# Kernel tuning notes

Hardware: AMD Instinct MI355X
Metric: run time of the kernel (lower is better)

Reference implementation:

```python
import jax, jax.numpy as jnp
import numpy as np

NUM_HEADS = 16
HEAD_DIM = 64
HIDDEN = NUM_HEADS * HEAD_DIM  # 1024


def get_rel_pos(q_size, k_size, rel_pos):
    # q_size == k_size here and rel_pos already has 2*size-1 rows, so the
    # F.interpolate(mode='linear') resize in the original is an identity.
    # relative_coords = q - k + (k_size - 1)  (scale factors are 1.0)
    coords = jnp.arange(q_size)[:, None] - jnp.arange(k_size)[None, :] + (k_size - 1)
    return rel_pos[coords]  # [q_size, k_size, head_dim]


def setup_inputs() -> dict:
    key = jax.random.key(0)
    ks = jax.random.split(key, 7)
    B, H, W = 4, 56, 28
    inp = {
        "hidden_states": jax.random.normal(ks[0], (B, H, W, HIDDEN), jnp.float32),
        "qkv_w": jax.random.normal(ks[1], (3 * HIDDEN, HIDDEN), jnp.float32) * 0.02,
        "qkv_b": jax.random.normal(ks[2], (3 * HIDDEN,), jnp.float32) * 0.02,
        "proj_w": jax.random.normal(ks[3], (HIDDEN, HIDDEN), jnp.float32) * 0.02,
        "proj_b": jax.random.normal(ks[4], (HIDDEN,), jnp.float32) * 0.02,
        "rel_pos_h": jax.random.normal(ks[5], (2 * H - 1, HEAD_DIM), jnp.float32) * 0.02,
        "rel_pos_w": jax.random.normal(ks[6], (2 * W - 1, HEAD_DIM), jnp.float32) * 0.02,
    }
    return inp


def reference(hidden_states, qkv_w, qkv_b, proj_w, proj_b, rel_pos_h, rel_pos_w):
    B, H, W, C = hidden_states.shape
    N = H * W
    scale = HEAD_DIM ** -0.5

    # qkv projection -> [3, B*heads, N, head_dim]
    qkv = hidden_states @ qkv_w.T + qkv_b
    qkv = qkv.reshape(B, N, 3, NUM_HEADS, HEAD_DIM).transpose(2, 0, 3, 1, 4)
    qkv = qkv.reshape(3, B * NUM_HEADS, N, HEAD_DIM)
    query, key_, value = qkv[0], qkv[1], qkv[2]

    # scaled dot-product scores, fully materialized as in the original
    attn = jnp.einsum('bqd,bkd->bqk', query * scale, key_)  # [B*heads, N, N]

    # decomposed relative position bias
    Rh = get_rel_pos(H, H, rel_pos_h)  # [H, H, d]
    Rw = get_rel_pos(W, W, rel_pos_w)  # [W, W, d]
    q_r = query.reshape(B * NUM_HEADS, H, W, HEAD_DIM)
    rel_h = jnp.einsum('bhwc,hkc->bhwk', q_r, Rh)  # [B*heads, H, W, H]
    rel_w = jnp.einsum('bhwc,wkc->bhwk', q_r, Rw)  # [B*heads, H, W, W]
    attn = attn.reshape(B * NUM_HEADS, H, W, H, W)
    attn = attn + rel_h[:, :, :, :, None] + rel_w[:, :, :, None, :]
    attn = attn.reshape(B * NUM_HEADS, N, N)

    attn = jax.nn.softmax(attn.astype(jnp.float32), axis=-1).astype(query.dtype)

    out = jnp.einsum('bqk,bkd->bqd', attn, value)
    out = out.reshape(B, NUM_HEADS, H, W, HEAD_DIM).transpose(0, 2, 3, 1, 4)
    out = out.reshape(B, H, W, C)
    out = out @ proj_w.T + proj_b
    return out
```

## Files before the change

kernel.cpp:

```cpp
#include <hip/hip_runtime.h>
#include <hip/hip_bf16.h>
#include <stdint.h>

typedef __bf16 bf16;
typedef __bf16 bf16x2 __attribute__((ext_vector_type(2)));
typedef __bf16 bf16x4 __attribute__((ext_vector_type(4)));
typedef __bf16 bf16x8 __attribute__((ext_vector_type(8)));
typedef float f32x4 __attribute__((ext_vector_type(4)));

#define AS1 __attribute__((address_space(1)))
#define AS3 __attribute__((address_space(3)))

static __device__ __forceinline__ void async_cp16(const bf16* g, bf16* l) {
    __builtin_amdgcn_global_load_lds((const AS1 void*)g, (AS3 void*)l, 16, 0, 0);
}

static __device__ __forceinline__ bf16x4 cvt4(f32x4 v) {
    bf16x4 r;
    r[0] = (bf16)v[0]; r[1] = (bf16)v[1]; r[2] = (bf16)v[2]; r[3] = (bf16)v[3];
    return r;
}

static __device__ __forceinline__ float fast_exp2(float x) {
#if __has_builtin(__builtin_amdgcn_exp2f)
    return __builtin_amdgcn_exp2f(x);
#else
    return __expf(x * 0.69314718056f);
#endif
}

__global__ __launch_bounds__(256) void cvt_kernel(
    const float* __restrict__ src, bf16* __restrict__ dst, int n4) {
    int i = blockIdx.x * 256 + threadIdx.x;
    const int stride = gridDim.x * 256;
    for (; i < n4; i += stride)
        ((bf16x4*)dst)[i] = cvt4(((const f32x4*)src)[i]);
}


#define QKV_EPILOGUE()                                                        \
    for (int nt = 0; nt < 4; nt++) {                                          \
        const int n_ = n0 + wn + nt * 16 + lm;                                \
        const float bv = bias[n_];                                            \
        const int s = n_ >> 10, rem = n_ & 1023;                              \
        const int h = rem >> 6, d = rem & 63;                                 \
        const float qsc = (s == 0) ? 0.18033688011112042f : 1.0f;             \
        for (int mt = 0; mt < 4; mt++) {                                      \
            for (int r = 0; r < 4; r++) {                                     \
                const int m_ = m0 + wm + mt * 16 + quad * 4 + r;              \
                const int b = m_ / 1568;                                      \
                const int pix = m_ - b * 1568;                                \
                const int g = b * 16 + h;                                     \
                const bf16 v = (bf16)((acc[mt][nt][r] + bv) * qsc);           \
                if (s == 0)      Qb[((size_t)g * 1568 + pix) * 64 + d] = v;   \
                else if (s == 1) Kb[((size_t)g * 1568 + pix) * 64 + d] = v;   \
                else {                                                        \
                    const int lk = pix & 31;                                  \
                    const int ppix = (pix & ~31) | ((lk & 15) << 1) | (lk >> 4); \
                    Vt[((size_t)g * 64 + d) * 1568 + ppix] = v;               \
                }                                                             \
            }                                                                 \
        }                                                                     \
    }

__global__ __launch_bounds__(256) void qkv_gemm_bf16(
    const bf16* __restrict__ A, const bf16* __restrict__ W,
    const float* __restrict__ bias, bf16* __restrict__ Qb,
    bf16* __restrict__ Kb, bf16* __restrict__ Vt) {
    __shared__ bf16 As[128 * 32];
    __shared__ bf16 Bs[128 * 32];
    const int t = threadIdx.x;
    const int wid = t >> 6, lane = t & 63;
    const int m0 = blockIdx.x * 128, n0 = blockIdx.y * 128;
    const int wm = (wid & 1) * 64, wn = (wid >> 1) * 64;
    const int r_i = lane >> 2, c8 = (lane & 3) * 8;
    const int lm = lane & 15, quad = lane >> 4;

    f32x4 acc[4][4] = {};
    for (int k0 = 0; k0 < 1024; k0 += 32) {
        __syncthreads();
        for (int i = 0; i < 2; i++) {
            const int blk = wid * 2 + i;
            async_cp16(A + (size_t)(m0 + blk * 16 + r_i) * 1024 + k0 + c8, As + blk * 512);
            async_cp16(W + (size_t)(n0 + blk * 16 + r_i) * 1024 + k0 + c8, Bs + blk * 512);
        }
        __syncthreads();
        bf16x8 af[4], bfr[4];
        for (int x = 0; x < 4; x++) {
            af[x]  = *(const bf16x8*)&As[(wm + x * 16 + lm) * 32 + quad * 8];
            bfr[x] = *(const bf16x8*)&Bs[(wn + x * 16 + lm) * 32 + quad * 8];
        }
        for (int mt = 0; mt < 4; mt++)
            for (int nt = 0; nt < 4; nt++)
                acc[mt][nt] = __builtin_amdgcn_mfma_f32_16x16x32_bf16(af[mt], bfr[nt], acc[mt][nt], 0, 0, 0);
    }
    QKV_EPILOGUE()
}

__global__ __launch_bounds__(256) void qkv_gemm_f32(
    const float* __restrict__ A, const float* __restrict__ W,
    const float* __restrict__ bias, bf16* __restrict__ Qb,
    bf16* __restrict__ Kb, bf16* __restrict__ Vt) {
    __shared__ bf16 As[128 * 32];
    __shared__ bf16 Bs[128 * 32];
    const int t = threadIdx.x;
    const int wid = t >> 6, lane = t & 63;
    const int m0 = blockIdx.x * 128, n0 = blockIdx.y * 128;
    const int wm = (wid & 1) * 64, wn = (wid >> 1) * 64;
    const int lm = lane & 15, quad = lane >> 4;

    f32x4 acc[4][4] = {};
    for (int k0 = 0; k0 < 1024; k0 += 32) {
        __syncthreads();
        for (int i = 0; i < 4; i++) {
            const int idx = t + i * 256;
            const int row = idx >> 3, c4 = (idx & 7) * 4;
            const f32x4 av = *(const f32x4*)&A[(size_t)(m0 + row) * 1024 + k0 + c4];
            const f32x4 wv = *(const f32x4*)&W[(size_t)(n0 + row) * 1024 + k0 + c4];
            *(bf16x4*)&As[row * 32 + c4] = cvt4(av);
            *(bf16x4*)&Bs[row * 32 + c4] = cvt4(wv);
        }
        __syncthreads();
        bf16x8 af[4], bfr[4];
        for (int x = 0; x < 4; x++) {
            af[x]  = *(const bf16x8*)&As[(wm + x * 16 + lm) * 32 + quad * 8];
            bfr[x] = *(const bf16x8*)&Bs[(wn + x * 16 + lm) * 32 + quad * 8];
        }
        for (int mt = 0; mt < 4; mt++)
            for (int nt = 0; nt < 4; nt++)
                acc[mt][nt] = __builtin_amdgcn_mfma_f32_16x16x32_bf16(af[mt], bfr[nt], acc[mt][nt], 0, 0, 0);
    }
    QKV_EPILOGUE()
}

__global__ __launch_bounds__(256) void flash_attn(
    const bf16* __restrict__ Qb, const bf16* __restrict__ Kb,
    const bf16* __restrict__ Vt, const float* __restrict__ rph,
    const float* __restrict__ rpw, bf16* __restrict__ AO) {
    const int x = blockIdx.x;
    const int xcd = x & 7, j = x >> 3;
    const int g = xcd * 8 + j / 25;
    const int qblk = j - (j / 25) * 25;
    const int q0 = qblk * 64;
    const int hqb = q0 / 28;

    __shared__ __align__(16) char smem[51712];
    float* Th = (float*)smem;
    float* Tw = (float*)(smem + 15360);
    const char* ThC = (const char*)smem;
    const char* TwC = (const char*)(smem + 15360);
    char* B   = smem + 30208;
    bf16* Qs  = (bf16*)B;
    bf16* RPs = (bf16*)B;
    char* KsC = B;
    char* VsC = B + 8192;
    bf16* Ps  = (bf16*)(B + 16384);

    const int t = threadIdx.x, wid = t >> 6, lane = t & 63;
    const int lm = lane & 15, quad = lane >> 4;
    const int qbase_l = wid * 16 + quad * 4;
    const int swz = (lm & 7) << 4;

    for (int c = t; c < 512; c += 256) {
        const int row = c >> 3, col = (c & 7) * 8;
        const int qg = min(q0 + row, 1567);
        *(bf16x8*)&Qs[row * 72 + col] =
            *(const bf16x8*)&Qb[((size_t)g * 1568 + qg) * 64 + col];
    }
    __syncthreads();
    const int qrow_l = wid * 16 + lm;
    const bf16x8 qf0 = *(const bf16x8*)&Qs[qrow_l * 72 + quad * 8];
    const bf16x8 qf1 = *(const bf16x8*)&Qs[qrow_l * 72 + 32 + quad * 8];

    int thbB[4], twbB[4];
#pragma unroll
    for (int r = 0; r < 4; r++) {
        const int qg = min(q0 + qbase_l + r, 1567);
        const int hq = qg / 28, wq = qg - hq * 28;
        thbB[r] = ((qbase_l + r) * 60 + (hq - hqb) + 55) * 4;
        twbB[r] = ((qbase_l + r) * 58 + wq + 27) * 4;
    }

    bf16x8 kreg[2], vreg[2];
#pragma unroll
    for (int i = 0; i < 2; i++) {
        const int idx = (i << 8) + t;
        kreg[i] = *(const bf16x8*)&Kb[((size_t)g * 1568 + (idx >> 3)) * 64 + ((idx & 7) << 3)];
        vreg[i] = *(const bf16x8*)&Vt[((size_t)g * 64 + (idx >> 3)) * 1568 + ((idx & 7) << 3)];
    }
    __syncthreads();

    for (int c = t; c < 1024; c += 256) {
        const int row = c >> 4, col = (c & 15) * 4;
        const int rg = min(hqb + row, 110);
        *(bf16x4*)&RPs[row * 72 + col] = cvt4(*(const f32x4*)&rph[rg * 64 + col]);
    }
    __syncthreads();
    f32x4 acch[4];
#pragma unroll
    for (int nt = 0; nt < 4; nt++) {
        const bf16x8 b0 = *(const bf16x8*)&RPs[(nt * 16 + lm) * 72 + quad * 8];
        const bf16x8 b1 = *(const bf16x8*)&RPs[(nt * 16 + lm) * 72 + 32 + quad * 8];
        f32x4 a = {};
        a = __builtin_amdgcn_mfma_f32_16x16x32_bf16(qf0, b0, a, 0, 0, 0);
        a = __builtin_amdgcn_mfma_f32_16x16x32_bf16(qf1, b1, a, 0, 0, 0);
        acch[nt] = a;
    }
    __syncthreads();

    for (int c = t; c < 1024; c += 256) {
        const int row = c >> 4, col = (c & 15) * 4;
        const int rg = min(row, 54);
        *(bf16x4*)&RPs[row * 72 + col] = cvt4(*(const f32x4*)&rpw[rg * 64 + col]);
    }
#pragma unroll
    for (int nt = 0; nt < 4; nt++) {
        const int c = nt * 16 + lm;
        if (c < 59) {
#pragma unroll
            for (int r = 0; r < 4; r++)
                Th[(qbase_l + r) * 60 + c] = acch[nt][r] * 8.0f - 14.4269504f;
        }
    }
    __syncthreads();
#pragma unroll
    for (int nt = 0; nt < 4; nt++) {
        const bf16x8 b0 = *(const bf16x8*)&RPs[(nt * 16 + lm) * 72 + quad * 8];
        const bf16x8 b1 = *(const bf16x8*)&RPs[(nt * 16 + lm) * 72 + 32 + quad * 8];
        f32x4 a = {};
        a = __builtin_amdgcn_mfma_f32_16x16x32_bf16(qf0, b0, a, 0, 0, 0);
        a = __builtin_amdgcn_mfma_f32_16x16x32_bf16(qf1, b1, a, 0, 0, 0);
        const int c = nt * 16 + lm;
        if (c < 55) {
#pragma unroll
            for (int r = 0; r < 4; r++)
                Tw[(qbase_l + r) * 58 + c] = a[r] * 8.0f;
        }
    }

    f32x4 o[4] = {};
    f32x4 lsum = {};
    bf16x8 ones;
#pragma unroll
    for (int i = 0; i < 8; i++) ones[i] = (bf16)1.0f;

    int hkB[4], wkB[4];
#pragma unroll
    for (int f = 0; f < 4; f++) {
        const int k = f * 16 + lm;
        const int hk = k / 28;
        hkB[f] = hk * 4;
        wkB[f] = (k - hk * 28) * 4;
    }
    bf16* Pw = &Ps[wid * 640];

    for (int kt = 0; kt < 25; kt++) {
        f32x4 s[4];
#pragma unroll
        for (int f = 0; f < 2; f++)
#pragma unroll
            for (int r = 0; r < 4; r++)
                s[f][r] = *(const float*)(ThC + (thbB[r] - hkB[f]))
                        + *(const float*)(TwC + (twbB[r] - wkB[f]));
        if (kt < 24) {
#pragma unroll
            for (int f = 2; f < 4; f++)
#pragma unroll
                for (int r = 0; r < 4; r++)
                    s[f][r] = *(const float*)(ThC + (thbB[r] - hkB[f]))
                            + *(const float*)(TwC + (twbB[r] - wkB[f]));
        } else {
#pragma unroll
            for (int f = 2; f < 4; f++)
#pragma unroll
                for (int r = 0; r < 4; r++)
                    s[f][r] = -30000.0f;
        }

        __syncthreads();
#pragma unroll
        for (int i = 0; i < 2; i++) {
            const int idx = (i << 8) + t;
            const int row = idx >> 3;
            const int cb = (((idx & 7) << 4) ^ ((row & 7) << 4));
            *(bf16x8*)(KsC + row * 128 + cb) = kreg[i];
            *(bf16x8*)(VsC + row * 128 + cb) = vreg[i];
        }
        {
            const int kb = min(kt + 1, 24) << 6;
#pragma unroll
            for (int i = 0; i < 2; i++) {
                const int idx = (i << 8) + t;
                const int krow = min(kb + (idx >> 3), 1567);
                kreg[i] = *(const bf16x8*)&Kb[((size_t)g * 1568 + krow) * 64 + ((idx & 7) << 3)];
                const int vcol = min(kb + ((idx & 7) << 3), 1560);
                vreg[i] = *(const bf16x8*)&Vt[((size_t)g * 64 + (idx >> 3)) * 1568 + vcol];
            }
        }
        __syncthreads();

        __builtin_amdgcn_s_setprio(1);
#pragma unroll
        for (int f = 0; f < 4; f++) {
            const char* rp = KsC + (f * 16 + lm) * 128;
            const int x0 = (quad * 16) ^ swz;
            const bf16x8 ka = *(const bf16x8*)(rp + x0);
            const bf16x8 kb2 = *(const bf16x8*)(rp + (x0 ^ 64));
            s[f] = __builtin_amdgcn_mfma_f32_16x16x32_bf16(qf0, ka, s[f], 0, 0, 0);
            s[f] = __builtin_amdgcn_mfma_f32_16x16x32_bf16(qf1, kb2, s[f], 0, 0, 0);
        }
        __builtin_amdgcn_s_setprio(0);

#pragma unroll
        for (int f = 0; f < 4; f++) {
            wkB[f] += 32; hkB[f] += 8;
            if (wkB[f] >= 112) { wkB[f] -= 112; hkB[f] += 4; }
        }

#pragma unroll
        for (int h = 0; h < 2; h++) {
#pragma unroll
            for (int r = 0; r < 4; r++) {
                const float p0 = fast_exp2(s[2 * h][r]);
                const float p1 = fast_exp2(s[2 * h + 1][r]);
                bf16x2 pp; pp[0] = (bf16)p0; pp[1] = (bf16)p1;
                *(bf16x2*)&Pw[(quad * 4 + r) * 40 + lm * 2] = pp;
            }
            __asm__ volatile("s_waitcnt lgkmcnt(0)" ::: "memory");
            const bf16x8 pf = *(const bf16x8*)&Pw[lm * 40 + quad * 8];
            lsum = __builtin_amdgcn_mfma_f32_16x16x32_bf16(pf, ones, lsum, 0, 0, 0);
            __builtin_amdgcn_s_setprio(1);
#pragma unroll
            for (int dt = 0; dt < 4; dt++) {
                const bf16x8 vf = *(const bf16x8*)(VsC + (dt * 16 + lm) * 128 +
                                                   (((h << 6) + quad * 16) ^ swz));
                o[dt] = __builtin_amdgcn_mfma_f32_16x16x32_bf16(pf, vf, o[dt], 0, 0, 0);
            }
            __builtin_amdgcn_s_setprio(0);
        }
    }

    if (q0 + wid * 16 < 1568) {
        const int bo = g >> 4, hh = g & 15;
#pragma unroll
        for (int r = 0; r < 4; r++) {
            const float inv = 1.0f / lsum[r];
            const size_t base = ((size_t)bo * 1568 + q0 + qbase_l + r) * 1024 + hh * 64;
#pragma unroll
            for (int dt = 0; dt < 4; dt++)
                AO[base + dt * 16 + lm] = (bf16)(o[dt][r] * inv);
        }
    }
}

__global__ __launch_bounds__(256) void proj_gemm_bf16(
    const bf16* __restrict__ A, const bf16* __restrict__ W,
    const float* __restrict__ bias, float* __restrict__ out) {
    __shared__ bf16 As[128 * 32];
    __shared__ bf16 Bs[128 * 32];
    const int t = threadIdx.x;
    const int wid = t >> 6, lane = t & 63;
    const int m0 = blockIdx.x * 128, n0 = blockIdx.y * 128;
    const int wm = (wid & 1) * 64, wn = (wid >> 1) * 64;
    const int r_i = lane >> 2, c8 = (lane & 3) * 8;
    const int lm = lane & 15, quad = lane >> 4;

    f32x4 acc[4][4] = {};
    for (int k0 = 0; k0 < 1024; k0 += 32) {
        __syncthreads();
        for (int i = 0; i < 2; i++) {
            const int blk = wid * 2 + i;
            async_cp16(A + (size_t)(m0 + blk * 16 + r_i) * 1024 + k0 + c8, As + blk * 512);
            async_cp16(W + (size_t)(n0 + blk * 16 + r_i) * 1024 + k0 + c8, Bs + blk * 512);
        }
        __syncthreads();
        bf16x8 af[4], bfr[4];
        for (int x = 0; x < 4; x++) {
            af[x]  = *(const bf16x8*)&As[(wm + x * 16 + lm) * 32 + quad * 8];
            bfr[x] = *(const bf16x8*)&Bs[(wn + x * 16 + lm) * 32 + quad * 8];
        }
        for (int mt = 0; mt < 4; mt++)
            for (int nt = 0; nt < 4; nt++)
                acc[mt][nt] = __builtin_amdgcn_mfma_f32_16x16x32_bf16(af[mt], bfr[nt], acc[mt][nt], 0, 0, 0);
    }
    for (int nt = 0; nt < 4; nt++) {
        const int n_ = n0 + wn + nt * 16 + lm;
        const float bv = bias[n_];
        for (int mt = 0; mt < 4; mt++)
            for (int r = 0; r < 4; r++) {
                const int m_ = m0 + wm + mt * 16 + quad * 4 + r;
                out[(size_t)m_ * 1024 + n_] = acc[mt][nt][r] + bv;
            }
    }
}

__global__ __launch_bounds__(256) void proj_gemm_f32(
    const bf16* __restrict__ A, const float* __restrict__ W,
    const float* __restrict__ bias, float* __restrict__ out) {
    __shared__ bf16 As[128 * 32];
    __shared__ bf16 Bs[128 * 32];
    const int t = threadIdx.x;
    const int wid = t >> 6, lane = t & 63;
    const int m0 = blockIdx.x * 128, n0 = blockIdx.y * 128;
    const int wm = (wid & 1) * 64, wn = (wid >> 1) * 64;
    const int r_i = lane >> 2, c8 = (lane & 3) * 8;
    const int lm = lane & 15, quad = lane >> 4;

    f32x4 acc[4][4] = {};
    for (int k0 = 0; k0 < 1024; k0 += 32) {
        __syncthreads();
        for (int i = 0; i < 2; i++) {
            const int blk = wid * 2 + i;
            async_cp16(A + (size_t)(m0 + blk * 16 + r_i) * 1024 + k0 + c8, As + blk * 512);
        }
        for (int i = 0; i < 4; i++) {
            const int idx = t + i * 256;
            const int row = idx >> 3, c4 = (idx & 7) * 4;
            const f32x4 wv = *(const f32x4*)&W[(size_t)(n0 + row) * 1024 + k0 + c4];
            *(bf16x4*)&Bs[row * 32 + c4] = cvt4(wv);
        }
        __syncthreads();
        bf16x8 af[4], bfr[4];
        for (int x = 0; x < 4; x++) {
            af[x]  = *(const bf16x8*)&As[(wm + x * 16 + lm) * 32 + quad * 8];
            bfr[x] = *(const bf16x8*)&Bs[(wn + x * 16 + lm) * 32 + quad * 8];
        }
        for (int mt = 0; mt < 4; mt++)
            for (int nt = 0; nt < 4; nt++)
                acc[mt][nt] = __builtin_amdgcn_mfma_f32_16x16x32_bf16(af[mt], bfr[nt], acc[mt][nt], 0, 0, 0);
    }
    for (int nt = 0; nt < 4; nt++) {
        const int n_ = n0 + wn + nt * 16 + lm;
        const float bv = bias[n_];
        for (int mt = 0; mt < 4; mt++)
            for (int r = 0; r < 4; r++) {
                const int m_ = m0 + wm + mt * 16 + quad * 4 + r;
                out[(size_t)m_ * 1024 + n_] = acc[mt][nt][r] + bv;
            }
    }
}

extern "C" void kernel_launch(void* const* d_in, const int* in_sizes, int n_in,
                              void* d_out, int out_size, void* d_ws, size_t ws_size,
                              hipStream_t stream) {
    const float* hs     = (const float*)d_in[0];
    const float* qkv_w  = (const float*)d_in[1];
    const float* qkv_b  = (const float*)d_in[2];
    const float* proj_w = (const float*)d_in[3];
    const float* proj_b = (const float*)d_in[4];
    const float* rph    = (const float*)d_in[5];
    const float* rpw    = (const float*)d_in[6];
    float* out = (float*)d_out;

    const size_t GQ = (size_t)64 * 1568 * 64;
    const size_t N_HS = (size_t)6272 * 1024;
    const size_t N_QW = (size_t)3072 * 1024;
    const size_t N_PW = (size_t)1024 * 1024;
    bf16* Qb = (bf16*)d_ws;
    bf16* Kb = Qb + GQ;
    bf16* Vt = Kb + GQ;
    bf16* AO = Vt + GQ;
    bf16* hs_bf    = AO + GQ;
    bf16* qkvw_bf  = hs_bf + N_HS;
    bf16* projw_bf = qkvw_bf + N_QW;
    const size_t need = (4 * GQ + N_HS + N_QW + N_PW) * sizeof(bf16);

    if (ws_size >= need) {
        cvt_kernel<<<512, 256, 0, stream>>>(hs, hs_bf, (int)(N_HS / 4));
        cvt_kernel<<<512, 256, 0, stream>>>(qkv_w, qkvw_bf, (int)(N_QW / 4));
        cvt_kernel<<<256, 256, 0, stream>>>(proj_w, projw_bf, (int)(N_PW / 4));
        qkv_gemm_bf16<<<dim3(49, 24), 256, 0, stream>>>(hs_bf, qkvw_bf, qkv_b, Qb, Kb, Vt);
        flash_attn<<<1600, 256, 0, stream>>>(Qb, Kb, Vt, rph, rpw, AO);
        proj_gemm_bf16<<<dim3(49, 8), 256, 0, stream>>>(AO, projw_bf, proj_b, out);
    } else {
        qkv_gemm_f32<<<dim3(49, 24), 256, 0, stream>>>(hs, qkv_w, qkv_b, Qb, Kb, Vt);
        flash_attn<<<1600, 256, 0, stream>>>(Qb, Kb, Vt, rph, rpw, AO);
        proj_gemm_f32<<<dim3(49, 8), 256, 0, stream>>>(AO, proj_w, proj_b, out);
    }
}
```

Before: 337.9 us.

## Compute relative-position bias via one-hot MFMA instead of LDS gathers

Replaces the per-element LDS gathers of the height and width relative-position tables with an extra MFMA per key fragment. A precomputed one-hot key matrix (Kone) selects the right bias from a per-query bf16 table holding 28 width entries plus 4 height entries. This moves scalar LDS loads and adds onto the matrix cores. In exchange, the bias is rounded to bf16, which costs some precision. It also adds a small setup kernel, an extra global and LDS stream per tile, and one more sync in the prologue.

```diff
diff --git a/kernel.cpp b/kernel.cpp
--- a/kernel.cpp
+++ b/kernel.cpp
@@ -35,6 +35,25 @@
     const int stride = gridDim.x * 256;
     for (; i < n4; i += stride)
         ((bf16x4*)dst)[i] = cvt4(((const f32x4*)src)[i]);
+}
+
+__global__ __launch_bounds__(256) void build_kone(bf16* __restrict__ Kone) {
+    const int idx = blockIdx.x * 256 + threadIdx.x;
+    if (idx >= 6400) return;
+    const int key = idx >> 2, chunk = idx & 3;
+    const int hk = key / 28;
+    const int wk = key - hk * 28;
+    const int kt = key >> 6;
+    const int ha = (kt << 6) / 28;
+    const int jw = 27 - wk;
+    const int jh = 31 - (hk - ha);
+    bf16x8 v;
+#pragma unroll
+    for (int e = 0; e < 8; e++) {
+        const int j = chunk * 8 + e;
+        v[e] = (j == jw || j == jh) ? (bf16)1.0f : (bf16)0.0f;
+    }
+    *(bf16x8*)&Kone[key * 32 + chunk * 8] = v;
 }
 
 
@@ -136,7 +155,8 @@
 __global__ __launch_bounds__(256) void flash_attn(
     const bf16* __restrict__ Qb, const bf16* __restrict__ Kb,
     const bf16* __restrict__ Vt, const float* __restrict__ rph,
-    const float* __restrict__ rpw, bf16* __restrict__ AO) {
+    const float* __restrict__ rpw, const bf16* __restrict__ Kone,
+    bf16* __restrict__ AO) {
     const int x = blockIdx.x;
     const int xcd = x & 7, j = x >> 3;
     const int g = xcd * 8 + j / 25;
@@ -144,17 +164,18 @@
     const int q0 = qblk * 64;
     const int hqb = q0 / 28;
 
-    __shared__ __align__(16) char smem[51712];
-    float* Th = (float*)smem;
-    float* Tw = (float*)(smem + 15360);
+    __shared__ __align__(16) char smem[45312];
+    float* Th  = (float*)smem;
     const char* ThC = (const char*)smem;
-    const char* TwC = (const char*)(smem + 15360);
-    char* B   = smem + 30208;
+    bf16* TwS = (bf16*)(smem + 15616);
+    char* B   = smem + 19712;
     bf16* Qs  = (bf16*)B;
     bf16* RPs = (bf16*)B;
+    float* TwF = (float*)(B + 9216);
     char* KsC = B;
     char* VsC = B + 8192;
-    bf16* Ps  = (bf16*)(B + 16384);
+    bf16* KoneS = (bf16*)(B + 16384);
+    bf16* Ps  = (bf16*)(B + 20480);
 
     const int t = threadIdx.x, wid = t >> 6, lane = t & 63;
     const int lm = lane & 15, quad = lane >> 4;
@@ -172,22 +193,18 @@
     const bf16x8 qf0 = *(const bf16x8*)&Qs[qrow_l * 72 + quad * 8];
     const bf16x8 qf1 = *(const bf16x8*)&Qs[qrow_l * 72 + 32 + quad * 8];
 
-    int thbB[4], twbB[4];
-#pragma unroll
-    for (int r = 0; r < 4; r++) {
-        const int qg = min(q0 + qbase_l + r, 1567);
-        const int hq = qg / 28, wq = qg - hq * 28;
-        thbB[r] = ((qbase_l + r) * 60 + (hq - hqb) + 55) * 4;
-        twbB[r] = ((qbase_l + r) * 58 + wq + 27) * 4;
-    }
-
-    bf16x8 kreg[2], vreg[2];
+    const int qgl = min(q0 + qrow_l, 1567);
+    const int thb2 = (qrow_l * 61 + (qgl / 28 - hqb) + 54) * 4;
+
+    const int kobase = ((t >> 2) << 5) + ((t & 3) << 3);
+    bf16x8 kreg[2], vreg[2], koreg;
 #pragma unroll
     for (int i = 0; i < 2; i++) {
         const int idx = (i << 8) + t;
         kreg[i] = *(const bf16x8*)&Kb[((size_t)g * 1568 + (idx >> 3)) * 64 + ((idx & 7) << 3)];
         vreg[i] = *(const bf16x8*)&Vt[((size_t)g * 64 + (idx >> 3)) * 1568 + ((idx & 7) << 3)];
     }
+    koreg = *(const bf16x8*)&Kone[kobase];
     __syncthreads();
 
     for (int c = t; c < 1024; c += 256) {
@@ -219,7 +236,7 @@
         if (c < 59) {
 #pragma unroll
             for (int r = 0; r < 4; r++)
-                Th[(qbase_l + r) * 60 + c] = acch[nt][r] * 8.0f - 14.4269504f;
+                Th[(qbase_l + r) * 61 + c + 2] = acch[nt][r] * 8.0f;
         }
     }
     __syncthreads();
@@ -234,48 +251,52 @@
         if (c < 55) {
 #pragma unroll
             for (int r = 0; r < 4; r++)
-                Tw[(qbase_l + r) * 58 + c] = a[r] * 8.0f;
-        }
-    }
+                TwF[(qbase_l + r) * 58 + c] = a[r] * 8.0f;
+        }
+    }
+    __syncthreads();
+
+    {
+        const int row = t >> 2, chunk = t & 3;
+        const int qg = min(q0 + row, 1567);
+        const int wq = qg % 28;
+        const float* src = &TwF[row * 58 + wq];
+        bf16x8 v;
+        if (chunk < 3) {
+#pragma unroll
+            for (int e = 0; e < 8; e++) v[e] = (bf16)src[chunk * 8 + e];
+        } else {
+#pragma unroll
+            for (int e = 0; e < 4; e++) v[e] = (bf16)src[24 + e];
+#pragma unroll
+            for (int e = 4; e < 8; e++) v[e] = (bf16)0.0f;
+        }
+        *(bf16x8*)&TwS[row * 32 + chunk * 8] = v;
+    }
+    __syncthreads();
+
+    const bf16x8 qt_mine = *(const bf16x8*)&TwS[qrow_l * 32 + quad * 8];
 
     f32x4 o[4] = {};
     f32x4 lsum = {};
+    const f32x4 zero4 = {};
     bf16x8 ones;
 #pragma unroll
     for (int i = 0; i < 8; i++) ones[i] = (bf16)1.0f;
 
-    int hkB[4], wkB[4];
-#pragma unroll
-    for (int f = 0; f < 4; f++) {
-        const int k = f * 16 + lm;
-        const int hk = k / 28;
-        hkB[f] = hk * 4;
-        wkB[f] = (k - hk * 28) * 4;
-    }
     bf16* Pw = &Ps[wid * 640];
 
     for (int kt = 0; kt < 25; kt++) {
-        f32x4 s[4];
-#pragma unroll
-        for (int f = 0; f < 2; f++)
-#pragma unroll
-            for (int r = 0; r < 4; r++)
-                s[f][r] = *(const float*)(ThC + (thbB[r] - hkB[f]))
-                        + *(const float*)(TwC + (twbB[r] - wkB[f]));
-        if (kt < 24) {
-#pragma unroll
-            for (int f = 2; f < 4; f++)
-#pragma unroll
-                for (int r = 0; r < 4; r++)
-                    s[f][r] = *(const float*)(ThC + (thbB[r] - hkB[f]))
-                            + *(const float*)(TwC + (twbB[r] - wkB[f]));
-        } else {
-#pragma unroll
-            for (int f = 2; f < 4; f++)
-#pragma unroll
-                for (int r = 0; r < 4; r++)
-                    s[f][r] = -30000.0f;
-        }
+        const int ha = (kt << 6) / 28;
+        const char* tp = ThC + (thb2 - (ha << 2));
+        const float w0 = *(const float*)(tp);
+        const float w1 = *(const float*)(tp + 4);
+        const float w2 = *(const float*)(tp + 8);
+        const float w3 = *(const float*)(tp + 12);
+        bf16x8 qmod = qt_mine;
+        qmod[4] = (bf16)w0; qmod[5] = (bf16)w1;
+        qmod[6] = (bf16)w2; qmod[7] = (bf16)w3;
+        const bf16x8 qf2 = (quad == 3) ? qmod : qt_mine;
 
         __syncthreads();
 #pragma unroll
@@ -286,8 +307,10 @@
             *(bf16x8*)(KsC + row * 128 + cb) = kreg[i];
             *(bf16x8*)(VsC + row * 128 + cb) = vreg[i];
         }
+        *(bf16x8*)&KoneS[kobase] = koreg;
         {
-            const int kb = min(kt + 1, 24) << 6;
+            const int ktn = min(kt + 1, 24);
+            const int kb = ktn << 6;
 #pragma unroll
             for (int i = 0; i < 2; i++) {
                 const int idx = (i << 8) + t;
@@ -296,10 +319,17 @@
                 const int vcol = min(kb + ((idx & 7) << 3), 1560);
                 vreg[i] = *(const bf16x8*)&Vt[((size_t)g * 64 + (idx >> 3)) * 1568 + vcol];
             }
+            koreg = *(const bf16x8*)&Kone[((size_t)ktn << 11) + kobase];
         }
         __syncthreads();
 
         __builtin_amdgcn_s_setprio(1);
+        f32x4 s[4];
+#pragma unroll
+        for (int f = 0; f < 4; f++) {
+            const bf16x8 ko = *(const bf16x8*)&KoneS[(f * 16 + lm) * 32 + quad * 8];
+            s[f] = __builtin_amdgcn_mfma_f32_16x16x32_bf16(qf2, ko, zero4, 0, 0, 0);
+        }
 #pragma unroll
         for (int f = 0; f < 4; f++) {
             const char* rp = KsC + (f * 16 + lm) * 128;
@@ -311,10 +341,9 @@
         }
         __builtin_amdgcn_s_setprio(0);
 
-#pragma unroll
-        for (int f = 0; f < 4; f++) {
-            wkB[f] += 32; hkB[f] += 8;
-            if (wkB[f] >= 112) { wkB[f] -= 112; hkB[f] += 4; }
+        if (kt == 24) {
+#pragma unroll
+            for (int r = 0; r < 4; r++) { s[2][r] = -30000.0f; s[3][r] = -30000.0f; }
         }
 
 #pragma unroll
@@ -453,6 +482,7 @@
     float* out = (float*)d_out;
 
     const size_t GQ = (size_t)64 * 1568 * 64;
+    const size_t N_KONE = (size_t)1600 * 32;
     const size_t N_HS = (size_t)6272 * 1024;
     const size_t N_QW = (size_t)3072 * 1024;
     const size_t N_PW = (size_t)1024 * 1024;
@@ -460,21 +490,24 @@
     bf16* Kb = Qb + GQ;
     bf16* Vt = Kb + GQ;
     bf16* AO = Vt + GQ;
-    bf16* hs_bf    = AO + GQ;
+    bf16* Kone = AO + GQ;
+    bf16* hs_bf    = Kone + N_KONE;
     bf16* qkvw_bf  = hs_bf + N_HS;
     bf16* projw_bf = qkvw_bf + N_QW;
-    const size_t need = (4 * GQ + N_HS + N_QW + N_PW) * sizeof(bf16);
+    const size_t need = (4 * GQ + N_KONE + N_HS + N_QW + N_PW) * sizeof(bf16);
 
     if (ws_size >= need) {
+        build_kone<<<25, 256, 0, stream>>>(Kone);
         cvt_kernel<<<512, 256, 0, stream>>>(hs, hs_bf, (int)(N_HS / 4));
         cvt_kernel<<<512, 256, 0, stream>>>(qkv_w, qkvw_bf, (int)(N_QW / 4));
         cvt_kernel<<<256, 256, 0, stream>>>(proj_w, projw_bf, (int)(N_PW / 4));
         qkv_gemm_bf16<<<dim3(49, 24), 256, 0, stream>>>(hs_bf, qkvw_bf, qkv_b, Qb, Kb, Vt);
-        flash_attn<<<1600, 256, 0, stream>>>(Qb, Kb, Vt, rph, rpw, AO);
+        flash_attn<<<1600, 256, 0, stream>>>(Qb, Kb, Vt, rph, rpw, Kone, AO);
         proj_gemm_bf16<<<dim3(49, 8), 256, 0, stream>>>(AO, projw_bf, proj_b, out);
     } else {
+        build_kone<<<25, 256, 0, stream>>>(Kone);
         qkv_gemm_f32<<<dim3(49, 24), 256, 0, stream>>>(hs, qkv_w, qkv_b, Qb, Kb, Vt);
-        flash_attn<<<1600, 256, 0, stream>>>(Qb, Kb, Vt, rph, rpw, AO);
+        flash_attn<<<1600, 256, 0, stream>>>(Qb, Kb, Vt, rph, rpw, Kone, AO);
         proj_gemm_f32<<<dim3(49, 8), 256, 0, stream>>>(AO, proj_w, proj_b, out);
     }
 }
```

After: 328.3 us. 1.03x faster.
